# Optimization experiments

Hardware: AMD Instinct MI355X
Metric: run time of the kernel (lower is better)

The kernel has to match this reference:

```python
import jax, jax.numpy as jnp
import numpy as np

HEADS = 4
DIM_HEAD = 32


def setup_inputs() -> dict:
    key = jax.random.key(0)
    k1, k2, k3 = jax.random.split(key, 3)
    B, L, D = 16, 8192, 256
    hidden = HEADS * DIM_HEAD  # 128
    x = jax.random.normal(k1, (B, L, D), dtype=jnp.float32)
    W_qkv = jax.random.normal(k2, (D, 3 * hidden), dtype=jnp.float32) * (D ** -0.5)
    W_out = jax.random.normal(k3, (hidden, D), dtype=jnp.float32) * (hidden ** -0.5)
    b_out = jnp.zeros((D,), dtype=jnp.float32)
    return {"x": x, "W_qkv": W_qkv, "W_out": W_out, "b_out": b_out}


def reference(x, W_qkv, W_out, b_out):
    B, L, D = x.shape
    scale = DIM_HEAD ** -0.5
    # 1x1 conv == per-token matmul
    qkv = jnp.einsum('bld,df->blf', x, W_qkv)  # [B, L, 3*h*dh]
    qkv = qkv.reshape(B, L, 3, HEADS, DIM_HEAD)
    q = jnp.transpose(qkv[:, :, 0], (0, 2, 1, 3)) * scale          # [B, h, L, d]
    k = jax.nn.softmax(jnp.transpose(qkv[:, :, 1], (0, 2, 1, 3)), axis=2)  # softmax over L
    v = jnp.transpose(qkv[:, :, 2], (0, 2, 1, 3))                  # [B, h, L, e]
    context = jnp.einsum('bhld,bhle->bhde', k, v)                  # [B, h, d, e]
    out = jnp.einsum('bhde,bhld->bhle', context, q)                # [B, h, L, e]
    out = jnp.transpose(out, (0, 2, 1, 3)).reshape(B, L, HEADS * DIM_HEAD)
    return jnp.einsum('blf,fd->bld', out, W_out) + b_out
```

## Files before the change

kernel.cpp:

```cpp
#include <hip/hip_runtime.h>
#include <math.h>


#define BL 131072

typedef __attribute__((ext_vector_type(8))) short bf16x8;
typedef __attribute__((ext_vector_type(4))) float f32x4;
typedef __attribute__((ext_vector_type(4))) unsigned u32x4;

__device__ __forceinline__ unsigned cvt_pk2(float a, float b) {
    unsigned r;
    asm("v_cvt_pk_bf16_f32 %0, %1, %2" : "=v"(r) : "v"(a), "v"(b));
    return r;
}
__device__ __forceinline__ ushort bf16_rn(float f) {
    return (ushort)cvt_pk2(f, f);
}
__device__ __forceinline__ float bf16f(ushort h) { return __uint_as_float(((unsigned)h) << 16); }

__device__ __forceinline__ void glds16(const void* g, void* l) {
    __builtin_amdgcn_global_load_lds((const __attribute__((address_space(1))) unsigned int*)g,
                                     (__attribute__((address_space(3))) unsigned int*)l,
                                     16, 0, 0);
}

__global__ __launch_bounds__(256) void init_stats(float* S, float* Z) {
    int i = blockIdx.x * 256 + threadIdx.x;
    if (i < 65536) S[i] = 0.f;
    if (i < 2048) Z[i] = 0.f;
}

__global__ __launch_bounds__(256) void convert_w(const float* __restrict__ W,
                                                 ushort* __restrict__ wh,
                                                 ushort* __restrict__ wl) {
    int n = blockIdx.x, k = threadIdx.x;
    float f = W[k * 384 + n];
    ushort h = bf16_rn(f);
    wh[n * 256 + k] = h;
    wl[n * 256 + k] = bf16_rn(f - bf16f(h));
}

__global__ __launch_bounds__(256) void gemm1_kernel(
    const float* __restrict__ X,
    const ushort* __restrict__ Wh, const ushort* __restrict__ Wl,
    ushort* __restrict__ Qh, ushort* __restrict__ Ql,
    float* __restrict__ KV) {
    __shared__ __align__(16) float  As[4096];
    __shared__ __align__(16) ushort Bsh[4096];
    __shared__ __align__(16) ushort Bsl[4096];
    const int tid = threadIdx.x;
    const int wg = blockIdx.x;
    const int xcd = wg & 7;
    const int slot = wg >> 3;
    const int cb = slot % 3;
    const int yb = (slot / 3) * 8 + xcd;
    const int col0 = cb * 128;
    const int row0 = yb * 128;
    const int lane = tid & 63, wave = tid >> 6;
    const int wr = (wave & 1) * 64, wc = (wave >> 1) * 64;
    const int m = lane & 15, quad = lane >> 4;
    const int ra = lane >> 3, pa = lane & 7;
    const int rb = lane >> 2, pb = lane & 3;

    f32x4 acc[4][4] = {};

    for (int k0 = 0; k0 < 256; k0 += 32) {
#pragma unroll
        for (int s = 0; s < 4; ++s) {
            int seg = s * 4 + wave;
            int r = seg * 8 + ra;
            int q = pa ^ (r & 7);
            glds16(&X[(long)(row0 + r) * 256 + k0 + q * 4], &As[seg * 256]);
        }
#pragma unroll
        for (int s = 0; s < 2; ++s) {
            int seg = s * 4 + wave;
            int r = seg * 16 + rb;
            int q = pb ^ ((r >> 1) & 3);
            glds16(&Wh[(long)(col0 + r) * 256 + k0 + q * 8], &Bsh[seg * 512]);
            glds16(&Wl[(long)(col0 + r) * 256 + k0 + q * 8], &Bsl[seg * 512]);
        }
        __syncthreads();

        bf16x8 bh[4], bl[4];
#pragma unroll
        for (int i = 0; i < 4; ++i) {
            int r = wc + i * 16 + m;
            int p = quad ^ ((r >> 1) & 3);
            bh[i] = *(const bf16x8*)&Bsh[r * 32 + p * 8];
            bl[i] = *(const bf16x8*)&Bsl[r * 32 + p * 8];
        }
#pragma unroll
        for (int i = 0; i < 4; ++i) {
            int r = wr + i * 16 + m;
            int p0 = (quad * 2) ^ (r & 7);
            int p1 = (quad * 2 + 1) ^ (r & 7);
            f32x4 a0 = *(const f32x4*)&As[r * 32 + p0 * 4];
            f32x4 a1 = *(const f32x4*)&As[r * 32 + p1 * 4];
            u32x4 ahw, alw;
#pragma unroll
            for (int e = 0; e < 2; ++e) {
                float f0 = a0[2 * e], f1 = a0[2 * e + 1];
                unsigned h = cvt_pk2(f0, f1);
                ahw[e] = h;
                alw[e] = cvt_pk2(f0 - __uint_as_float(h << 16),
                                 f1 - __uint_as_float(h & 0xFFFF0000u));
            }
#pragma unroll
            for (int e = 0; e < 2; ++e) {
                float f0 = a1[2 * e], f1 = a1[2 * e + 1];
                unsigned h = cvt_pk2(f0, f1);
                ahw[2 + e] = h;
                alw[2 + e] = cvt_pk2(f0 - __uint_as_float(h << 16),
                                     f1 - __uint_as_float(h & 0xFFFF0000u));
            }
            bf16x8 ah = __builtin_bit_cast(bf16x8, ahw);
            bf16x8 al = __builtin_bit_cast(bf16x8, alw);
#pragma unroll
            for (int j = 0; j < 4; ++j) {
                acc[i][j] = __builtin_amdgcn_mfma_f32_16x16x32_bf16(ah, bh[j], acc[i][j], 0, 0, 0);
                acc[i][j] = __builtin_amdgcn_mfma_f32_16x16x32_bf16(ah, bl[j], acc[i][j], 0, 0, 0);
                acc[i][j] = __builtin_amdgcn_mfma_f32_16x16x32_bf16(al, bh[j], acc[i][j], 0, 0, 0);
            }
        }
        __syncthreads();
    }

    if (cb == 0) {
#pragma unroll
        for (int i = 0; i < 4; ++i)
#pragma unroll
            for (int r4 = 0; r4 < 4; ++r4) {
                long row = row0 + wr + i * 16 + quad * 4 + r4;
#pragma unroll
                for (int j = 0; j < 4; ++j) {
                    float v = acc[i][j][r4];
                    int col = wc + j * 16 + m;
                    ushort h = bf16_rn(v);
                    Qh[row * 128 + col] = h;
                    Ql[row * 128 + col] = bf16_rn(v - bf16f(h));
                }
            }
    } else {
        int vofs = (cb == 2) ? 32 : 0;
#pragma unroll
        for (int i = 0; i < 4; ++i)
#pragma unroll
            for (int r4 = 0; r4 < 4; ++r4) {
                long row = row0 + wr + i * 16 + quad * 4 + r4;
                long b = row >> 13, l = row & 8191;
#pragma unroll
                for (int j = 0; j < 4; ++j) {
                    int c = wc + j * 16 + m;
                    int h = c >> 5, dd = c & 31;
                    KV[(((b * 4 + h) * 8192 + l) * 64) + vofs + dd] = acc[i][j][r4];
                }
            }
    }
}

__global__ __launch_bounds__(256) void ksum_hb(const float* __restrict__ KV,
                                               float* __restrict__ S,
                                               float* __restrict__ Z) {
    int bx = blockIdx.x;
    int c = bx & 7, bh = bx >> 3;
    const float* slab = KV + ((long)bh * 8192 + c * 1024) * 64;
    __shared__ float tile[64][68];
    const int tid = threadIdx.x;
    const int dcol = tid & 31;
    const int e0 = (tid >> 5) * 4;
    const int c4 = tid & 15, lrow = tid >> 4;
    float z = 0.f;
    f32x4 acc = {0.f, 0.f, 0.f, 0.f};

    for (int t0 = 0; t0 < 1024; t0 += 64) {
#pragma unroll
        for (int u = 0; u < 4; ++u) {
            int l = u * 16 + lrow;
            float4 w = *(const float4*)&slab[((long)(t0 + l)) * 64 + c4 * 4];
            if (c4 < 8) { w.x = __expf(w.x); w.y = __expf(w.y); w.z = __expf(w.z); w.w = __expf(w.w); }
            *(float4*)&tile[l][c4 * 4] = w;
        }
        __syncthreads();
#pragma unroll 8
        for (int l = 0; l < 64; ++l) {
            float e = tile[l][dcol];
            f32x4 vv = *(const f32x4*)&tile[l][32 + e0];
            z += e;
            acc[0] += e * vv[0]; acc[1] += e * vv[1];
            acc[2] += e * vv[2]; acc[3] += e * vv[3];
        }
        __syncthreads();
    }
    if (tid < 32) atomicAdd(&Z[bh * 32 + dcol], z);
#pragma unroll
    for (int j = 0; j < 4; ++j)
        atomicAdd(&S[((long)bh * 32 + dcol) * 32 + e0 + j], acc[j]);
}

__global__ __launch_bounds__(256) void combine_kernel(const float* __restrict__ S,
                                                      const float* __restrict__ Z,
                                                      const float* __restrict__ Wout,
                                                      ushort* __restrict__ m2h,
                                                      ushort* __restrict__ m2l) {
    int bh = blockIdx.x;
    int b = bh >> 2, h = bh & 3;
    int n = threadIdx.x;
    __shared__ float ctx[32][32];
    __shared__ float zs[32];
    if (n < 32) zs[n] = Z[bh * 32 + n];
    __syncthreads();
#pragma unroll
    for (int t = 0; t < 4; ++t) {
        int idx = t * 256 + n;
        int d = idx >> 5, e = idx & 31;
        ctx[d][e] = S[(long)bh * 1024 + idx] / zs[d];
    }
    __syncthreads();
    const float scale = 0.17677669529663687f;
    float acc[32];
#pragma unroll
    for (int d = 0; d < 32; ++d) acc[d] = 0.f;
    for (int e = 0; e < 32; ++e) {
        float w = Wout[(h * 32 + e) * 256 + n];
#pragma unroll
        for (int d = 0; d < 32; ++d) acc[d] += ctx[d][e] * w;
    }
#pragma unroll
    for (int d = 0; d < 32; ++d) {
        float v = acc[d] * scale;
        long idx = ((long)(b * 256 + n)) * 128 + h * 32 + d;
        ushort hh = bf16_rn(v);
        m2h[idx] = hh;
        m2l[idx] = bf16_rn(v - bf16f(hh));
    }
}

__global__ __launch_bounds__(256) void gemm2_kernel(
    const ushort* __restrict__ Ahp, const ushort* __restrict__ Alp,
    const ushort* __restrict__ Bhp, const ushort* __restrict__ Blp,
    const float* __restrict__ bias, float* __restrict__ out) {
    __shared__ __align__(16) ushort Ash[4096];
    __shared__ __align__(16) ushort Asl[4096];
    __shared__ __align__(16) ushort Bsh[4096];
    __shared__ __align__(16) ushort Bsl[4096];
    const int tid = threadIdx.x;
    const int col0 = blockIdx.x * 128;
    const int row0 = blockIdx.y * 128;
    const long bz = blockIdx.z;
    const ushort* Ah = Ahp + bz * (8192L * 128);
    const ushort* Al = Alp + bz * (8192L * 128);
    const ushort* Bh = Bhp + bz * (256L * 128);
    const ushort* Bl = Blp + bz * (256L * 128);
    const int lane = tid & 63, wave = tid >> 6;
    const int wr = (wave & 1) * 64, wc = (wave >> 1) * 64;
    const int m = lane & 15, quad = lane >> 4;
    const int rb = lane >> 2, pb = lane & 3;

    f32x4 acc[4][4] = {};

    for (int k0 = 0; k0 < 128; k0 += 32) {
#pragma unroll
        for (int s = 0; s < 2; ++s) {
            int seg = s * 4 + wave;
            int r = seg * 16 + rb;
            int q = pb ^ ((r >> 1) & 3);
            glds16(&Ah[(long)(row0 + r) * 128 + k0 + q * 8], &Ash[seg * 512]);
            glds16(&Al[(long)(row0 + r) * 128 + k0 + q * 8], &Asl[seg * 512]);
            glds16(&Bh[(long)(col0 + r) * 128 + k0 + q * 8], &Bsh[seg * 512]);
            glds16(&Bl[(long)(col0 + r) * 128 + k0 + q * 8], &Bsl[seg * 512]);
        }
        __syncthreads();

        bf16x8 af[2][4], bg[2][4];
#pragma unroll
        for (int i = 0; i < 4; ++i) {
            int rA = wr + i * 16 + m;
            int pA = quad ^ ((rA >> 1) & 3);
            af[0][i] = *(const bf16x8*)&Ash[rA * 32 + pA * 8];
            af[1][i] = *(const bf16x8*)&Asl[rA * 32 + pA * 8];
            int rB = wc + i * 16 + m;
            int pB = quad ^ ((rB >> 1) & 3);
            bg[0][i] = *(const bf16x8*)&Bsh[rB * 32 + pB * 8];
            bg[1][i] = *(const bf16x8*)&Bsl[rB * 32 + pB * 8];
        }
#pragma unroll
        for (int i = 0; i < 4; ++i)
#pragma unroll
            for (int j = 0; j < 4; ++j) {
                acc[i][j] = __builtin_amdgcn_mfma_f32_16x16x32_bf16(af[0][i], bg[0][j], acc[i][j], 0, 0, 0);
                acc[i][j] = __builtin_amdgcn_mfma_f32_16x16x32_bf16(af[0][i], bg[1][j], acc[i][j], 0, 0, 0);
                acc[i][j] = __builtin_amdgcn_mfma_f32_16x16x32_bf16(af[1][i], bg[0][j], acc[i][j], 0, 0, 0);
            }
        __syncthreads();
    }

    float bv[4];
#pragma unroll
    for (int j = 0; j < 4; ++j) bv[j] = bias[col0 + wc + j * 16 + m];
    float* outb = out + bz * (8192L * 256);
#pragma unroll
    for (int i = 0; i < 4; ++i)
#pragma unroll
        for (int r4 = 0; r4 < 4; ++r4) {
            long row = row0 + wr + i * 16 + quad * 4 + r4;
#pragma unroll
            for (int j = 0; j < 4; ++j)
                outb[row * 256 + col0 + wc + j * 16 + m] = acc[i][j][r4] + bv[j];
        }
}

extern "C" void kernel_launch(void* const* d_in, const int* in_sizes, int n_in,
                              void* d_out, int out_size, void* d_ws, size_t ws_size,
                              hipStream_t stream) {
    const float* x     = (const float*)d_in[0];
    const float* W_qkv = (const float*)d_in[1];
    const float* W_out = (const float*)d_in[2];
    const float* b_out = (const float*)d_in[3];
    float* out = (float*)d_out;

    char* p = (char*)d_ws;
    float* kv   = (float*)p;  p += (long)64 * 8192 * 64 * 4;
    float* S    = (float*)p;  p += 65536 * 4;
    float* Z    = (float*)p;  p += 2048 * 4;
    ushort* wth = (ushort*)p; p += 384 * 256 * 2;
    ushort* wtl = (ushort*)p; p += 384 * 256 * 2;
    ushort* qh  = (ushort*)p; p += (long)BL * 128 * 2;
    ushort* ql  = (ushort*)p; p += (long)BL * 128 * 2;
    ushort* m2h = (ushort*)p; p += 16 * 256 * 128 * 2;
    ushort* m2l = (ushort*)p; p += 16 * 256 * 128 * 2;

    init_stats<<<264, 256, 0, stream>>>(S, Z);
    convert_w<<<384, 256, 0, stream>>>(W_qkv, wth, wtl);

    gemm1_kernel<<<3072, 256, 0, stream>>>(x, wth, wtl, qh, ql, kv);

    ksum_hb<<<512, 256, 0, stream>>>(kv, S, Z);
    combine_kernel<<<64, 256, 0, stream>>>(S, Z, W_out, m2h, m2l);

    gemm2_kernel<<<dim3(2, 64, 16), 256, 0, stream>>>(qh, ql, m2h, m2l, b_out, out);
}
```

Baseline: 431.3 us.

## Fold Q projection into per-batch effective output weight and fuse K/V reduction

Computes only the K and V projections, fusing exp and the context reduction into the GEMM epilogue through per-block partial sums instead of materialising KV and Q in global memory. The per-batch context and W_out are combined with the Q slice of W_qkv into an effective 256x256 weight per batch, so the final GEMM reads x directly. This removes the Q and KV round trips and the atomics. In exchange it adds a partial-sum buffer, a serial 128-way reduction in combine, and a precision change from folding the weights.

```diff
diff --git a/kernel.cpp b/kernel.cpp
--- a/kernel.cpp
+++ b/kernel.cpp
@@ -1,8 +1,6 @@
 #include <hip/hip_runtime.h>
 #include <math.h>
 
-
-#define BL 131072
 
 typedef __attribute__((ext_vector_type(8))) short bf16x8;
 typedef __attribute__((ext_vector_type(4))) float f32x4;
@@ -24,38 +22,224 @@
                                      16, 0, 0);
 }
 
-__global__ __launch_bounds__(256) void init_stats(float* S, float* Z) {
-    int i = blockIdx.x * 256 + threadIdx.x;
-    if (i < 65536) S[i] = 0.f;
-    if (i < 2048) Z[i] = 0.f;
-}
-
-__global__ __launch_bounds__(256) void convert_w(const float* __restrict__ W,
-                                                 ushort* __restrict__ wh,
-                                                 ushort* __restrict__ wl) {
+__global__ __launch_bounds__(256) void prep_kernel(const float* __restrict__ W,
+                                                   ushort* __restrict__ wh,
+                                                   ushort* __restrict__ wl) {
     int n = blockIdx.x, k = threadIdx.x;
-    float f = W[k * 384 + n];
+    float f = W[k * 384 + 128 + n];
     ushort h = bf16_rn(f);
     wh[n * 256 + k] = h;
     wl[n * 256 + k] = bf16_rn(f - bf16f(h));
 }
 
-__global__ __launch_bounds__(256) void gemm1_kernel(
+__global__ __launch_bounds__(256) void gemm_kv(
     const float* __restrict__ X,
     const ushort* __restrict__ Wh, const ushort* __restrict__ Wl,
-    ushort* __restrict__ Qh, ushort* __restrict__ Ql,
-    float* __restrict__ KV) {
+    float* __restrict__ S_part, float* __restrict__ Z_part) {
+    __shared__ __align__(16) char smem[66560];
+    float*  As  = (float*)smem;
+    ushort* Bsh = (ushort*)(smem + 8192);
+    ushort* Bsl = (ushort*)(smem + 8192 + 16384);
+    float*  tile = (float*)smem;
+
+    const int tid = threadIdx.x;
+    const int blk = blockIdx.x;
+    const long row0 = (long)blk * 64;
+    const int lane = tid & 63, wave = tid >> 6;
+    const int wc = wave * 64;
+    const int m = lane & 15, quad = lane >> 4;
+    const int ra = lane >> 3, pa = lane & 7;
+    const int rb = lane >> 2, pb = lane & 3;
+
+    f32x4 acc[4][4] = {};
+
+    for (int k0 = 0; k0 < 256; k0 += 32) {
+#pragma unroll
+        for (int s = 0; s < 2; ++s) {
+            int seg = s * 4 + wave;
+            int r = seg * 8 + ra;
+            int q = pa ^ (r & 7);
+            glds16(&X[(row0 + r) * 256 + k0 + q * 4], &As[seg * 256]);
+        }
+#pragma unroll
+        for (int s = 0; s < 4; ++s) {
+            int seg = s * 4 + wave;
+            int r = seg * 16 + rb;
+            int q = pb ^ ((r >> 1) & 3);
+            glds16(&Wh[r * 256 + k0 + q * 8], &Bsh[seg * 512]);
+            glds16(&Wl[r * 256 + k0 + q * 8], &Bsl[seg * 512]);
+        }
+        __syncthreads();
+
+        bf16x8 bh[4], bl[4];
+#pragma unroll
+        for (int j = 0; j < 4; ++j) {
+            int r = wc + j * 16 + m;
+            int p = quad ^ ((r >> 1) & 3);
+            bh[j] = *(const bf16x8*)&Bsh[r * 32 + p * 8];
+            bl[j] = *(const bf16x8*)&Bsl[r * 32 + p * 8];
+        }
+#pragma unroll
+        for (int i = 0; i < 4; ++i) {
+            int r = i * 16 + m;
+            int p0 = (quad * 2) ^ (r & 7);
+            int p1 = (quad * 2 + 1) ^ (r & 7);
+            f32x4 a0 = *(const f32x4*)&As[r * 32 + p0 * 4];
+            f32x4 a1 = *(const f32x4*)&As[r * 32 + p1 * 4];
+            u32x4 ahw, alw;
+#pragma unroll
+            for (int e = 0; e < 2; ++e) {
+                float f0 = a0[2 * e], f1 = a0[2 * e + 1];
+                unsigned h = cvt_pk2(f0, f1);
+                ahw[e] = h;
+                alw[e] = cvt_pk2(f0 - __uint_as_float(h << 16),
+                                 f1 - __uint_as_float(h & 0xFFFF0000u));
+            }
+#pragma unroll
+            for (int e = 0; e < 2; ++e) {
+                float f0 = a1[2 * e], f1 = a1[2 * e + 1];
+                unsigned h = cvt_pk2(f0, f1);
+                ahw[2 + e] = h;
+                alw[2 + e] = cvt_pk2(f0 - __uint_as_float(h << 16),
+                                     f1 - __uint_as_float(h & 0xFFFF0000u));
+            }
+            bf16x8 ah = __builtin_bit_cast(bf16x8, ahw);
+            bf16x8 al = __builtin_bit_cast(bf16x8, alw);
+#pragma unroll
+            for (int j = 0; j < 4; ++j) {
+                acc[i][j] = __builtin_amdgcn_mfma_f32_16x16x32_bf16(ah, bh[j], acc[i][j], 0, 0, 0);
+                acc[i][j] = __builtin_amdgcn_mfma_f32_16x16x32_bf16(ah, bl[j], acc[i][j], 0, 0, 0);
+                acc[i][j] = __builtin_amdgcn_mfma_f32_16x16x32_bf16(al, bh[j], acc[i][j], 0, 0, 0);
+            }
+        }
+        __syncthreads();
+    }
+
+#pragma unroll
+    for (int i = 0; i < 4; ++i)
+#pragma unroll
+        for (int r4 = 0; r4 < 4; ++r4) {
+            int rl = i * 16 + quad * 4 + r4;
+#pragma unroll
+            for (int j = 0; j < 4; ++j) {
+                int c = wc + j * 16 + m;
+                float v = acc[i][j][r4];
+                tile[rl * 260 + c] = (c < 128) ? __expf(v) : v;
+            }
+        }
+    __syncthreads();
+
+    const int h = wave, d = lane >> 1, eg = lane & 1, e0 = eg * 16;
+    float sacc[16] = {};
+    float z = 0.f;
+#pragma unroll 4
+    for (int l = 0; l < 64; ++l) {
+        const float* rowp = &tile[l * 260];
+        float ek = rowp[h * 32 + d];
+        const f32x4* vp = (const f32x4*)&rowp[128 + h * 32 + e0];
+        f32x4 v0 = vp[0], v1 = vp[1], v2 = vp[2], v3 = vp[3];
+        z += ek;
+        sacc[0]  += ek * v0[0]; sacc[1]  += ek * v0[1]; sacc[2]  += ek * v0[2]; sacc[3]  += ek * v0[3];
+        sacc[4]  += ek * v1[0]; sacc[5]  += ek * v1[1]; sacc[6]  += ek * v1[2]; sacc[7]  += ek * v1[3];
+        sacc[8]  += ek * v2[0]; sacc[9]  += ek * v2[1]; sacc[10] += ek * v2[2]; sacc[11] += ek * v2[3];
+        sacc[12] += ek * v3[0]; sacc[13] += ek * v3[1]; sacc[14] += ek * v3[2]; sacc[15] += ek * v3[3];
+    }
+    long sb = (long)blk * 4096 + h * 1024 + d * 32 + e0;
+#pragma unroll
+    for (int t = 0; t < 16; ++t) S_part[sb + t] = sacc[t];
+    if (eg == 0) Z_part[blk * 128 + h * 32 + d] = z;
+}
+
+__global__ __launch_bounds__(256) void combine_kernel(const float* __restrict__ S_part,
+                                                      const float* __restrict__ Z_part,
+                                                      const float* __restrict__ Wout,
+                                                      float* __restrict__ m2f) {
+    int bh = blockIdx.x;
+    int b = bh >> 2, h = bh & 3;
+    int n = threadIdx.x;
+    __shared__ float ctx[32][33];
+    __shared__ float zs[32];
+    if (n < 32) {
+        float z = 0.f;
+        for (int j = 0; j < 128; ++j) z += Z_part[(b * 128 + j) * 128 + h * 32 + n];
+        zs[n] = z;
+    }
+    float s4[4] = {};
+    for (int j = 0; j < 128; ++j) {
+        const float* sp = &S_part[((long)(b * 128 + j)) * 4096 + h * 1024];
+#pragma unroll
+        for (int t = 0; t < 4; ++t) s4[t] += sp[t * 256 + n];
+    }
+    __syncthreads();
+#pragma unroll
+    for (int t = 0; t < 4; ++t) {
+        int idx = t * 256 + n;
+        ctx[idx >> 5][idx & 31] = s4[t] / zs[idx >> 5];
+    }
+    __syncthreads();
+    const float scale = 0.17677669529663687f;
+    float acc[32];
+#pragma unroll
+    for (int dd = 0; dd < 32; ++dd) acc[dd] = 0.f;
+    for (int e = 0; e < 32; ++e) {
+        float w = Wout[(h * 32 + e) * 256 + n];
+#pragma unroll
+        for (int dd = 0; dd < 32; ++dd) acc[dd] += ctx[dd][e] * w;
+    }
+#pragma unroll
+    for (int dd = 0; dd < 32; ++dd)
+        m2f[((long)(b * 128 + h * 32 + dd)) * 256 + n] = acc[dd] * scale;
+}
+
+__global__ __launch_bounds__(256) void w2eff_kernel(const float* __restrict__ Wqkv,
+                                                    const float* __restrict__ m2f,
+                                                    ushort* __restrict__ w2h,
+                                                    ushort* __restrict__ w2l) {
+    int bid = blockIdx.x;
+    int b = bid >> 4, kg = bid & 15;
+    int n = threadIdx.x;
+    __shared__ float lWq[16 * 128];
+#pragma unroll
+    for (int u = 0; u < 8; ++u) {
+        int idx = u * 256 + n;
+        int k = idx >> 7, hd = idx & 127;
+        lWq[idx] = Wqkv[(kg * 16 + k) * 384 + hd];
+    }
+    __syncthreads();
+    float acc[16] = {};
+    for (int hd = 0; hd < 128; ++hd) {
+        float mm = m2f[((long)(b * 128 + hd)) * 256 + n];
+#pragma unroll
+        for (int k = 0; k < 16; ++k) acc[k] += lWq[k * 128 + hd] * mm;
+    }
+    long base = ((long)(b * 256 + n)) * 256 + kg * 16;
+#pragma unroll
+    for (int k = 0; k < 16; ++k) {
+        ushort hh = bf16_rn(acc[k]);
+        w2h[base + k] = hh;
+        w2l[base + k] = bf16_rn(acc[k] - bf16f(hh));
+    }
+}
+
+__global__ __launch_bounds__(256) void gemm2_kernel(
+    const float* __restrict__ X,
+    const ushort* __restrict__ W2h, const ushort* __restrict__ W2l,
+    const float* __restrict__ bias, float* __restrict__ out) {
     __shared__ __align__(16) float  As[4096];
     __shared__ __align__(16) ushort Bsh[4096];
     __shared__ __align__(16) ushort Bsl[4096];
     const int tid = threadIdx.x;
     const int wg = blockIdx.x;
     const int xcd = wg & 7;
-    const int slot = wg >> 3;
-    const int cb = slot % 3;
-    const int yb = (slot / 3) * 8 + xcd;
-    const int col0 = cb * 128;
-    const int row0 = yb * 128;
+    const int u = wg >> 3;
+    const int cbl = u & 1;
+    const int gid = (u >> 1) * 8 + xcd;
+    const long bz = gid >> 6;
+    const int row0 = (gid & 63) * 128;
+    const int col0 = cbl * 128;
+    const float* Xb = X + bz * (8192L * 256);
+    const ushort* Bh = W2h + bz * (256L * 256);
+    const ushort* Bl = W2l + bz * (256L * 256);
     const int lane = tid & 63, wave = tid >> 6;
     const int wr = (wave & 1) * 64, wc = (wave >> 1) * 64;
     const int m = lane & 15, quad = lane >> 4;
@@ -70,25 +254,25 @@
             int seg = s * 4 + wave;
             int r = seg * 8 + ra;
             int q = pa ^ (r & 7);
-            glds16(&X[(long)(row0 + r) * 256 + k0 + q * 4], &As[seg * 256]);
+            glds16(&Xb[(long)(row0 + r) * 256 + k0 + q * 4], &As[seg * 256]);
         }
 #pragma unroll
         for (int s = 0; s < 2; ++s) {
             int seg = s * 4 + wave;
             int r = seg * 16 + rb;
             int q = pb ^ ((r >> 1) & 3);
-            glds16(&Wh[(long)(col0 + r) * 256 + k0 + q * 8], &Bsh[seg * 512]);
-            glds16(&Wl[(long)(col0 + r) * 256 + k0 + q * 8], &Bsl[seg * 512]);
+            glds16(&Bh[(col0 + r) * 256 + k0 + q * 8], &Bsh[seg * 512]);
+            glds16(&Bl[(col0 + r) * 256 + k0 + q * 8], &Bsl[seg * 512]);
         }
         __syncthreads();
 
         bf16x8 bh[4], bl[4];
 #pragma unroll
-        for (int i = 0; i < 4; ++i) {
-            int r = wc + i * 16 + m;
+        for (int j = 0; j < 4; ++j) {
+            int r = wc + j * 16 + m;
             int p = quad ^ ((r >> 1) & 3);
-            bh[i] = *(const bf16x8*)&Bsh[r * 32 + p * 8];
-            bl[i] = *(const bf16x8*)&Bsl[r * 32 + p * 8];
+            bh[j] = *(const bf16x8*)&Bsh[r * 32 + p * 8];
+            bl[j] = *(const bf16x8*)&Bsl[r * 32 + p * 8];
         }
 #pragma unroll
         for (int i = 0; i < 4; ++i) {
@@ -123,175 +307,6 @@
                 acc[i][j] = __builtin_amdgcn_mfma_f32_16x16x32_bf16(al, bh[j], acc[i][j], 0, 0, 0);
             }
         }
-        __syncthreads();
-    }
-
-    if (cb == 0) {
-#pragma unroll
-        for (int i = 0; i < 4; ++i)
-#pragma unroll
-            for (int r4 = 0; r4 < 4; ++r4) {
-                long row = row0 + wr + i * 16 + quad * 4 + r4;
-#pragma unroll
-                for (int j = 0; j < 4; ++j) {
-                    float v = acc[i][j][r4];
-                    int col = wc + j * 16 + m;
-                    ushort h = bf16_rn(v);
-                    Qh[row * 128 + col] = h;
-                    Ql[row * 128 + col] = bf16_rn(v - bf16f(h));
-                }
-            }
-    } else {
-        int vofs = (cb == 2) ? 32 : 0;
-#pragma unroll
-        for (int i = 0; i < 4; ++i)
-#pragma unroll
-            for (int r4 = 0; r4 < 4; ++r4) {
-                long row = row0 + wr + i * 16 + quad * 4 + r4;
-                long b = row >> 13, l = row & 8191;
-#pragma unroll
-                for (int j = 0; j < 4; ++j) {
-                    int c = wc + j * 16 + m;
-                    int h = c >> 5, dd = c & 31;
-                    KV[(((b * 4 + h) * 8192 + l) * 64) + vofs + dd] = acc[i][j][r4];
-                }
-            }
-    }
-}
-
-__global__ __launch_bounds__(256) void ksum_hb(const float* __restrict__ KV,
-                                               float* __restrict__ S,
-                                               float* __restrict__ Z) {
-    int bx = blockIdx.x;
-    int c = bx & 7, bh = bx >> 3;
-    const float* slab = KV + ((long)bh * 8192 + c * 1024) * 64;
-    __shared__ float tile[64][68];
-    const int tid = threadIdx.x;
-    const int dcol = tid & 31;
-    const int e0 = (tid >> 5) * 4;
-    const int c4 = tid & 15, lrow = tid >> 4;
-    float z = 0.f;
-    f32x4 acc = {0.f, 0.f, 0.f, 0.f};
-
-    for (int t0 = 0; t0 < 1024; t0 += 64) {
-#pragma unroll
-        for (int u = 0; u < 4; ++u) {
-            int l = u * 16 + lrow;
-            float4 w = *(const float4*)&slab[((long)(t0 + l)) * 64 + c4 * 4];
-            if (c4 < 8) { w.x = __expf(w.x); w.y = __expf(w.y); w.z = __expf(w.z); w.w = __expf(w.w); }
-            *(float4*)&tile[l][c4 * 4] = w;
-        }
-        __syncthreads();
-#pragma unroll 8
-        for (int l = 0; l < 64; ++l) {
-            float e = tile[l][dcol];
-            f32x4 vv = *(const f32x4*)&tile[l][32 + e0];
-            z += e;
-            acc[0] += e * vv[0]; acc[1] += e * vv[1];
-            acc[2] += e * vv[2]; acc[3] += e * vv[3];
-        }
-        __syncthreads();
-    }
-    if (tid < 32) atomicAdd(&Z[bh * 32 + dcol], z);
-#pragma unroll
-    for (int j = 0; j < 4; ++j)
-        atomicAdd(&S[((long)bh * 32 + dcol) * 32 + e0 + j], acc[j]);
-}
-
-__global__ __launch_bounds__(256) void combine_kernel(const float* __restrict__ S,
-                                                      const float* __restrict__ Z,
-                                                      const float* __restrict__ Wout,
-                                                      ushort* __restrict__ m2h,
-                                                      ushort* __restrict__ m2l) {
-    int bh = blockIdx.x;
-    int b = bh >> 2, h = bh & 3;
-    int n = threadIdx.x;
-    __shared__ float ctx[32][32];
-    __shared__ float zs[32];
-    if (n < 32) zs[n] = Z[bh * 32 + n];
-    __syncthreads();
-#pragma unroll
-    for (int t = 0; t < 4; ++t) {
-        int idx = t * 256 + n;
-        int d = idx >> 5, e = idx & 31;
-        ctx[d][e] = S[(long)bh * 1024 + idx] / zs[d];
-    }
-    __syncthreads();
-    const float scale = 0.17677669529663687f;
-    float acc[32];
-#pragma unroll
-    for (int d = 0; d < 32; ++d) acc[d] = 0.f;
-    for (int e = 0; e < 32; ++e) {
-        float w = Wout[(h * 32 + e) * 256 + n];
-#pragma unroll
-        for (int d = 0; d < 32; ++d) acc[d] += ctx[d][e] * w;
-    }
-#pragma unroll
-    for (int d = 0; d < 32; ++d) {
-        float v = acc[d] * scale;
-        long idx = ((long)(b * 256 + n)) * 128 + h * 32 + d;
-        ushort hh = bf16_rn(v);
-        m2h[idx] = hh;
-        m2l[idx] = bf16_rn(v - bf16f(hh));
-    }
-}
-
-__global__ __launch_bounds__(256) void gemm2_kernel(
-    const ushort* __restrict__ Ahp, const ushort* __restrict__ Alp,
-    const ushort* __restrict__ Bhp, const ushort* __restrict__ Blp,
-    const float* __restrict__ bias, float* __restrict__ out) {
-    __shared__ __align__(16) ushort Ash[4096];
-    __shared__ __align__(16) ushort Asl[4096];
-    __shared__ __align__(16) ushort Bsh[4096];
-    __shared__ __align__(16) ushort Bsl[4096];
-    const int tid = threadIdx.x;
-    const int col0 = blockIdx.x * 128;
-    const int row0 = blockIdx.y * 128;
-    const long bz = blockIdx.z;
-    const ushort* Ah = Ahp + bz * (8192L * 128);
-    const ushort* Al = Alp + bz * (8192L * 128);
-    const ushort* Bh = Bhp + bz * (256L * 128);
-    const ushort* Bl = Blp + bz * (256L * 128);
-    const int lane = tid & 63, wave = tid >> 6;
-    const int wr = (wave & 1) * 64, wc = (wave >> 1) * 64;
-    const int m = lane & 15, quad = lane >> 4;
-    const int rb = lane >> 2, pb = lane & 3;
-
-    f32x4 acc[4][4] = {};
-
-    for (int k0 = 0; k0 < 128; k0 += 32) {
-#pragma unroll
-        for (int s = 0; s < 2; ++s) {
-            int seg = s * 4 + wave;
-            int r = seg * 16 + rb;
-            int q = pb ^ ((r >> 1) & 3);
-            glds16(&Ah[(long)(row0 + r) * 128 + k0 + q * 8], &Ash[seg * 512]);
-            glds16(&Al[(long)(row0 + r) * 128 + k0 + q * 8], &Asl[seg * 512]);
-            glds16(&Bh[(long)(col0 + r) * 128 + k0 + q * 8], &Bsh[seg * 512]);
-            glds16(&Bl[(long)(col0 + r) * 128 + k0 + q * 8], &Bsl[seg * 512]);
-        }
-        __syncthreads();
-
-        bf16x8 af[2][4], bg[2][4];
-#pragma unroll
-        for (int i = 0; i < 4; ++i) {
-            int rA = wr + i * 16 + m;
-            int pA = quad ^ ((rA >> 1) & 3);
-            af[0][i] = *(const bf16x8*)&Ash[rA * 32 + pA * 8];
-            af[1][i] = *(const bf16x8*)&Asl[rA * 32 + pA * 8];
-            int rB = wc + i * 16 + m;
-            int pB = quad ^ ((rB >> 1) & 3);
-            bg[0][i] = *(const bf16x8*)&Bsh[rB * 32 + pB * 8];
-            bg[1][i] = *(const bf16x8*)&Bsl[rB * 32 + pB * 8];
-        }
-#pragma unroll
-        for (int i = 0; i < 4; ++i)
-#pragma unroll
-            for (int j = 0; j < 4; ++j) {
-                acc[i][j] = __builtin_amdgcn_mfma_f32_16x16x32_bf16(af[0][i], bg[0][j], acc[i][j], 0, 0, 0);
-                acc[i][j] = __builtin_amdgcn_mfma_f32_16x16x32_bf16(af[0][i], bg[1][j], acc[i][j], 0, 0, 0);
-                acc[i][j] = __builtin_amdgcn_mfma_f32_16x16x32_bf16(af[1][i], bg[0][j], acc[i][j], 0, 0, 0);
-            }
         __syncthreads();
     }
 
@@ -320,23 +335,17 @@
     float* out = (float*)d_out;
 
     char* p = (char*)d_ws;
-    float* kv   = (float*)p;  p += (long)64 * 8192 * 64 * 4;
-    float* S    = (float*)p;  p += 65536 * 4;
-    float* Z    = (float*)p;  p += 2048 * 4;
-    ushort* wth = (ushort*)p; p += 384 * 256 * 2;
-    ushort* wtl = (ushort*)p; p += 384 * 256 * 2;
-    ushort* qh  = (ushort*)p; p += (long)BL * 128 * 2;
-    ushort* ql  = (ushort*)p; p += (long)BL * 128 * 2;
-    ushort* m2h = (ushort*)p; p += 16 * 256 * 128 * 2;
-    ushort* m2l = (ushort*)p; p += 16 * 256 * 128 * 2;
-
-    init_stats<<<264, 256, 0, stream>>>(S, Z);
-    convert_w<<<384, 256, 0, stream>>>(W_qkv, wth, wtl);
-
-    gemm1_kernel<<<3072, 256, 0, stream>>>(x, wth, wtl, qh, ql, kv);
-
-    ksum_hb<<<512, 256, 0, stream>>>(kv, S, Z);
-    combine_kernel<<<64, 256, 0, stream>>>(S, Z, W_out, m2h, m2l);
-
-    gemm2_kernel<<<dim3(2, 64, 16), 256, 0, stream>>>(qh, ql, m2h, m2l, b_out, out);
-}
+    ushort* wth = (ushort*)p; p += 256 * 256 * 2;
+    ushort* wtl = (ushort*)p; p += 256 * 256 * 2;
+    float* Sp   = (float*)p;  p += (long)2048 * 4096 * 4;
+    float* Zp   = (float*)p;  p += 2048 * 128 * 4;
+    float* m2f  = (float*)p;  p += 16 * 128 * 256 * 4;
+    ushort* w2h = (ushort*)p; p += (long)16 * 256 * 256 * 2;
+    ushort* w2l = (ushort*)p; p += (long)16 * 256 * 256 * 2;
+
+    prep_kernel<<<256, 256, 0, stream>>>(W_qkv, wth, wtl);
+    gemm_kv<<<2048, 256, 0, stream>>>(x, wth, wtl, Sp, Zp);
+    combine_kernel<<<64, 256, 0, stream>>>(Sp, Zp, W_out, m2f);
+    w2eff_kernel<<<256, 256, 0, stream>>>(W_qkv, m2f, w2h, w2l);
+    gemm2_kernel<<<2048, 256, 0, stream>>>(x, w2h, w2l, b_out, out);
+}
```

Result: faster. 382.1 us (-11.4%).
